# Performance work log

Hardware: AMD Instinct MI355X
Metric: run time of the kernel (lower is better)

Reference implementation:

```python
import jax, jax.numpy as jnp
import numpy as np

HEAD, SIZE = 16, 64
DIM = HEAD * SIZE
NINF = -10000.0
EPS = 1e-6


def setup_inputs() -> dict:
    key = jax.random.key(0)
    ks = jax.random.split(key, 12)
    B, S = 4, 2048
    std = 0.02
    return {
        "x": jax.random.normal(ks[0], (B, S, DIM), jnp.float32),
        "mask": jax.random.randint(ks[1], (B, S), 0, 2, jnp.int32),
        "wq_w": jax.random.normal(ks[2], (DIM, DIM), jnp.float32) * std,
        "wq_b": jnp.zeros((DIM,), jnp.float32),
        "wk_w": jax.random.normal(ks[3], (DIM, DIM), jnp.float32) * std,
        "wk_b": jnp.zeros((DIM,), jnp.float32),
        "wv_w": jax.random.normal(ks[4], (DIM, DIM), jnp.float32) * std,
        "wv_b": jnp.zeros((DIM,), jnp.float32),
        "dense_w": jax.random.normal(ks[5], (DIM, DIM), jnp.float32) * std,
        "dense_b": jnp.zeros((DIM,), jnp.float32),
        "gamma": jnp.ones((DIM,), jnp.float32),
        "beta": jnp.zeros((DIM,), jnp.float32),
    }


def _split_heads(t):
    # [B, S, DIM] -> [B, H, S, size]
    B, S, _ = t.shape
    return t.reshape(B, S, HEAD, SIZE).transpose(0, 2, 1, 3)


def _layernorm(x, gamma, beta):
    mu = jnp.mean(x, axis=-1, keepdims=True)
    var = jnp.mean(jnp.square(x - mu), axis=-1, keepdims=True)
    return (x - mu) * jax.lax.rsqrt(var + EPS) * gamma + beta


def reference(x, mask, wq_w, wq_b, wk_w, wk_b, wv_w, wv_b, dense_w, dense_b, gamma, beta):
    B, S, _ = x.shape
    q = _split_heads(x @ wq_w + wq_b)
    k = _split_heads(x @ wk_w + wk_b)
    v = _split_heads(x @ wv_w + wv_b)
    # scores [B, H, S, S]
    scores = jnp.einsum("bhqd,bhkd->bhqk", q, k) / jnp.sqrt(jnp.float32(SIZE))
    scores = scores + mask.astype(jnp.float32)[:, None, None, :] * NINF
    attn = jax.nn.softmax(scores, axis=-1)
    ctx = jnp.einsum("bhqk,bhkd->bhqd", attn, v)  # [B, H, S, size]
    ctx = ctx.transpose(0, 2, 1, 3).reshape(B, S, DIM)
    out = _layernorm(x + (ctx @ dense_w + dense_b), gamma, beta)
    return out, attn
```

## Files before the change

kernel.cpp:

```cpp
#include <hip/hip_runtime.h>
#include <stdint.h>

#define NB 4
#define NS 2048
#define NH 16
#define HSZ 64
#define ND 1024
#define NM (NB*NS)
#define QSCALE 0.180336880f
#define MADD2 -14426.950409f

typedef unsigned short u16;
typedef unsigned int u32;
typedef __attribute__((ext_vector_type(4))) float f32x4;
typedef __attribute__((ext_vector_type(8))) __bf16 bf16x8;

static __device__ __forceinline__ u16 f2bf(float f){
  unsigned int x = __builtin_bit_cast(unsigned int, f);
  x += 0x7fffu + ((x >> 16) & 1u);
  return (u16)(x >> 16);
}
static __device__ __forceinline__ u16 f2bf_rz(float f){
  return (u16)(__builtin_bit_cast(unsigned int, f) >> 16);
}

#define GLDS16(gp, lp) __builtin_amdgcn_global_load_lds( \
    (const __attribute__((address_space(1))) void*)(gp),  \
    (__attribute__((address_space(3))) void*)(lp), 16, 0, 0)

__global__ __launch_bounds__(256) void k_cast(const float4* __restrict__ in,
                                              ushort4* __restrict__ out, int n4){
  int i = blockIdx.x*256 + threadIdx.x;
  if (i >= n4) return;
  float4 v = in[i];
  ushort4 o;
  o.x = f2bf(v.x); o.y = f2bf(v.y); o.z = f2bf(v.z); o.w = f2bf(v.w);
  out[i] = o;
}

__global__ __launch_bounds__(256) void k_transpose4(const float* __restrict__ wq,
    const float* __restrict__ wk, const float* __restrict__ wv,
    const float* __restrict__ wd, u16* __restrict__ wcat, u16* __restrict__ wdt){
  __shared__ float t[32][33];
  const int z = blockIdx.z;
  const float* in = (z==0) ? wq : (z==1) ? wk : (z==2) ? wv : wd;
  u16* out = (z<3) ? (wcat + (size_t)z*ND*ND) : wdt;
  int tx = threadIdx.x & 31, ty = threadIdx.x >> 5;
  int n0 = blockIdx.x*32, k0 = blockIdx.y*32;
  #pragma unroll
  for (int i=0;i<32;i+=8)
    t[ty+i][tx] = in[(size_t)(k0+ty+i)*ND + n0 + tx];
  __syncthreads();
  #pragma unroll
  for (int i=0;i<32;i+=8)
    out[(size_t)(n0+ty+i)*ND + k0 + tx] = f2bf(t[tx][ty+i]);
}

template<int EPI>
__global__ __launch_bounds__(256,2) void k_gemm(const u16* __restrict__ A,
    const u16* __restrict__ Bt, const float* __restrict__ b0,
    const float* __restrict__ b1, const float* __restrict__ b2,
    const float* __restrict__ resid, u16* __restrict__ Qo, u16* __restrict__ Ko,
    u16* __restrict__ Vto, float* __restrict__ Out){
  __shared__ u16 sA[128*64];
  __shared__ u16 sB[128*64];
  const int tid = threadIdx.x;
  const int wave = tid >> 6, lane = tid & 63;
  const int l15 = lane & 15, l4 = lane >> 4;
  const int m0 = blockIdx.x * 128, n0 = blockIdx.y * 128;
  const int wm = wave >> 1, wn = wave & 1;
  const f32x4 vz = {0.f,0.f,0.f,0.f};
  f32x4 acc[4][4];
  #pragma unroll
  for (int i=0;i<4;i++)
    #pragma unroll
    for (int j=0;j<4;j++) acc[i][j] = vz;

  for (int k0 = 0; k0 < 1024; k0 += 64){
    __syncthreads();
    #pragma unroll
    for (int t=0; t<4; t++){
      const int jb = (t*4 + wave)*64;
      const int j  = jb + lane;
      const int r = j >> 3, c = (j & 7) << 3;
      GLDS16(A  + (((size_t)(m0 + r)) << 10) + (size_t)(k0 + c), sA + jb*8);
      GLDS16(Bt + (((size_t)(n0 + r)) << 10) + (size_t)(k0 + c), sB + jb*8);
    }
    __syncthreads();
    #pragma unroll
    for (int kk=0; kk<64; kk+=32){
      bf16x8 af[4], bv[4];
      #pragma unroll
      for (int mi=0;mi<4;mi++)
        af[mi] = *(const bf16x8*)(const void*)(sA + (wm*64 + mi*16 + l15)*64 + kk + l4*8);
      #pragma unroll
      for (int ni=0;ni<4;ni++)
        bv[ni] = *(const bf16x8*)(const void*)(sB + (wn*64 + ni*16 + l15)*64 + kk + l4*8);
      #pragma unroll
      for (int mi=0;mi<4;mi++)
        #pragma unroll
        for (int ni=0;ni<4;ni++)
          acc[mi][ni] = __builtin_amdgcn_mfma_f32_16x16x32_bf16(af[mi], bv[ni], acc[mi][ni], 0, 0, 0);
    }
  }

  if (EPI == 0){
    const int sec = n0 >> 10;
    const float* bias = (sec==0) ? b0 : (sec==1) ? b1 : b2;
    const float scale = (sec==0) ? QSCALE : 1.0f;
    u16* dst = (sec==0) ? Qo : (sec==1) ? Ko : Vto;
    #pragma unroll
    for (int mi=0;mi<4;mi++){
      #pragma unroll
      for (int ni=0;ni<4;ni++){
        const int n = n0 + wn*64 + ni*16 + l15;
        const int nn = n & (ND-1);
        const int h = nn >> 6, d = nn & 63;
        const float bvv = bias[nn];
        #pragma unroll
        for (int j=0;j<4;j++){
          const int m = m0 + wm*64 + mi*16 + l4*4 + j;
          const int b = m >> 11, s = m & (NS-1);
          const float v = (acc[mi][ni][j] + bvv) * scale;
          if (sec < 2)
            dst[((((size_t)b*NH + h)*NS + s) << 6) + d] = f2bf(v);
          else
            dst[((((size_t)b*NH + h)*HSZ + d) << 11) + s] = f2bf(v);
        }
      }
    }
  } else {
    #pragma unroll
    for (int mi=0;mi<4;mi++){
      #pragma unroll
      for (int ni=0;ni<4;ni++){
        const int n = n0 + wn*64 + ni*16 + l15;
        const float bvv = b0[n];
        #pragma unroll
        for (int j=0;j<4;j++){
          const int m = m0 + wm*64 + mi*16 + l4*4 + j;
          const size_t o = ((size_t)m << 10) + n;
          Out[o] = acc[mi][ni][j] + bvv + resid[o];
        }
      }
    }
  }
}

static __device__ __forceinline__ void attn_decode(int bid, int& qb, int& bh){
  const int x = bid & 7, t = bid >> 3;
  qb = t & 15;
  bh = (t >> 4) * 8 + x;
}
static __device__ __forceinline__ void attn_decode8(int bid, int& qb, int& bh){
  const int x = bid & 7, t = bid >> 3;
  qb = t & 7;
  bh = (t >> 3) * 8 + x;
}

__global__ __launch_bounds__(512,4) void k_attn_stats(const u16* __restrict__ Q,
    const u16* __restrict__ K, const int* __restrict__ mask,
    float* __restrict__ stats){
  __shared__ u16 sK[2][64][72];
  __shared__ float sMadd[NS];
  const int tid = threadIdx.x, wave = tid>>6, lane = tid&63;
  const int l15 = lane&15, l4 = lane>>4;
  int qb, bh; attn_decode8(blockIdx.x, qb, bh);
  const int b = bh >> 4;
  const size_t hoff = (size_t)bh * NS * HSZ;
  const int q0 = qb*256 + wave*32;
  const u16* Kg = K + hoff;
  bf16x8 qf0[2], qf1[2];
  #pragma unroll
  for (int m=0;m<2;m++){
    qf0[m] = *(const bf16x8*)(const void*)(Q + hoff + (size_t)(q0+m*16+l15)*HSZ + l4*8);
    qf1[m] = *(const bf16x8*)(const void*)(Q + hoff + (size_t)(q0+m*16+l15)*HSZ + 32 + l4*8);
  }
  const f32x4 vz = {0.f,0.f,0.f,0.f};
  const int r = tid >> 3, c = (tid & 7) << 3;
  float lr[2][4] = {{0.f,0.f,0.f,0.f},{0.f,0.f,0.f,0.f}};

  #pragma unroll
  for (int t=0;t<4;t++){
    const int kk = t*512 + tid;
    sMadd[kk] = mask[b*NS + kk] ? MADD2 : 0.f;
  }
  int4 rK = *(const int4*)(const void*)(Kg + (size_t)r*HSZ + c);
  *(int4*)(void*)&sK[0][r][c] = rK;
  rK = *(const int4*)(const void*)(Kg + (size_t)(64+r)*HSZ + c);
  __syncthreads();

  for (int kb=0; kb<NS; kb+=64){
    const int cur = (kb>>6)&1;
    if (kb+64 < NS)
      *(int4*)(void*)&sK[cur^1][r][c] = rK;
    if (kb+128 < NS)
      rK = *(const int4*)(const void*)(Kg + (size_t)(kb+128+r)*HSZ + c);
    #pragma unroll
    for (int n=0;n<4;n++){
      bf16x8 kf0 = *(const bf16x8*)(const void*)&sK[cur][n*16+l15][l4*8];
      bf16x8 kf1 = *(const bf16x8*)(const void*)&sK[cur][n*16+l15][32+l4*8];
      const float madd = sMadd[kb + n*16 + l15];
      #pragma unroll
      for (int m=0;m<2;m++){
        f32x4 a = vz;
        a = __builtin_amdgcn_mfma_f32_16x16x32_bf16(qf0[m], kf0, a, 0,0,0);
        a = __builtin_amdgcn_mfma_f32_16x16x32_bf16(qf1[m], kf1, a, 0,0,0);
        #pragma unroll
        for (int j=0;j<4;j++)
          lr[m][j] += __builtin_amdgcn_exp2f(a[j] + madd);
      }
    }
    __syncthreads();
  }
  #pragma unroll
  for (int m=0;m<2;m++)
    #pragma unroll
    for (int j=0;j<4;j++){
      float l = lr[m][j];
      #pragma unroll
      for (int off=1; off<16; off<<=1)
        l += __shfl_xor(l, off, 64);
      if (l15 == 0)
        stats[(size_t)bh*NS + q0 + m*16 + l4*4 + j] = 1.f/l;
    }
}

__global__ __launch_bounds__(512,4) void k_attn_pv(const u16* __restrict__ Q,
    const u16* __restrict__ K, const u16* __restrict__ Vt,
    const int* __restrict__ mask, const float* __restrict__ stats,
    float* __restrict__ attn, u16* __restrict__ ctx){
  __shared__ u16 sK[2][64][72];
  __shared__ u16 sV[2][64][72];
  __shared__ u16 sP[8][16][72];
  __shared__ float sMadd[NS];
  const int tid = threadIdx.x, wave = tid>>6, lane = tid&63;
  const int l15 = lane&15, l4 = lane>>4;
  int qb, bh; attn_decode(blockIdx.x, qb, bh);
  const int b = bh >> 4, h = bh & 15;
  const size_t hoff = (size_t)bh * NS * HSZ;
  const int q0 = qb*128 + wave*16;
  const u16* Kg = K + hoff;
  const u16* Vg = Vt + hoff;
  const bf16x8 qf0 = *(const bf16x8*)(const void*)(Q + hoff + (size_t)(q0+l15)*HSZ + l4*8);
  const bf16x8 qf1 = *(const bf16x8*)(const void*)(Q + hoff + (size_t)(q0+l15)*HSZ + 32 + l4*8);
  float rinv[4];
  #pragma unroll
  for (int j=0;j<4;j++)
    rinv[j] = stats[(size_t)bh*NS + q0 + l4*4 + j];
  const f32x4 vz = {0.f,0.f,0.f,0.f};
  f32x4 cacc[4];
  #pragma unroll
  for (int i=0;i<4;i++) cacc[i] = vz;
  float* attn_base = attn + (size_t)bh * NS * NS;
  const int r = tid >> 3, c = (tid & 7) << 3;

  #pragma unroll
  for (int t=0;t<4;t++){
    const int kk = t*512 + tid;
    sMadd[kk] = mask[b*NS + kk] ? MADD2 : 0.f;
  }
  int4 rK = *(const int4*)(const void*)(Kg + (size_t)r*HSZ + c);
  int4 rV = *(const int4*)(const void*)(Vg + (size_t)r*NS + c);
  *(int4*)(void*)&sK[0][r][c] = rK;
  *(int4*)(void*)&sV[0][r][c] = rV;
  rK = *(const int4*)(const void*)(Kg + (size_t)(64+r)*HSZ + c);
  rV = *(const int4*)(const void*)(Vg + (size_t)r*NS + 64 + c);
  __syncthreads();

  for (int kb=0; kb<NS; kb+=64){
    const int cur = (kb>>6)&1;
    if (kb+64 < NS){
      *(int4*)(void*)&sK[cur^1][r][c] = rK;
      *(int4*)(void*)&sV[cur^1][r][c] = rV;
    }
    if (kb+128 < NS){
      rK = *(const int4*)(const void*)(Kg + (size_t)(kb+128+r)*HSZ + c);
      rV = *(const int4*)(const void*)(Vg + (size_t)r*NS + (kb+128) + c);
    }
    #pragma unroll
    for (int n=0;n<4;n++){
      bf16x8 kf0 = *(const bf16x8*)(const void*)&sK[cur][n*16+l15][l4*8];
      bf16x8 kf1 = *(const bf16x8*)(const void*)&sK[cur][n*16+l15][32+l4*8];
      f32x4 a = vz;
      a = __builtin_amdgcn_mfma_f32_16x16x32_bf16(qf0, kf0, a, 0,0,0);
      a = __builtin_amdgcn_mfma_f32_16x16x32_bf16(qf1, kf1, a, 0,0,0);
      const float madd = sMadd[kb + n*16 + l15];
      #pragma unroll
      for (int j=0;j<4;j++){
        const float e = __builtin_amdgcn_exp2f(a[j] + madd);
        sP[wave][l4*4+j][n*16+l15] = f2bf_rz(e * rinv[j]);
      }
    }
    #pragma unroll
    for (int kk=0;kk<2;kk++){
      bf16x8 pf = *(const bf16x8*)(const void*)&sP[wave][l15][kk*32 + l4*8];
      #pragma unroll
      for (int n2=0;n2<4;n2++){
        bf16x8 vf = *(const bf16x8*)(const void*)&sV[cur][n2*16+l15][kk*32 + l4*8];
        cacc[n2] = __builtin_amdgcn_mfma_f32_16x16x32_bf16(pf, vf, cacc[n2], 0,0,0);
      }
    }
    #pragma unroll
    for (int jj=0;jj<4;jj++){
      const int rr = jj*4 + l4;
      const uint2 pw = *(const uint2*)(const void*)&sP[wave][rr][l15*4];
      f32x4 o;
      o.x = __builtin_bit_cast(float, pw.x << 16);
      o.y = __builtin_bit_cast(float, pw.x & 0xffff0000u);
      o.z = __builtin_bit_cast(float, pw.y << 16);
      o.w = __builtin_bit_cast(float, pw.y & 0xffff0000u);
      __builtin_nontemporal_store(o,
          (f32x4*)(void*)&attn_base[(size_t)(q0 + rr)*NS + kb + l15*4]);
    }
    __syncthreads();
  }
  #pragma unroll
  for (int n2=0;n2<4;n2++)
    #pragma unroll
    for (int j=0;j<4;j++){
      const int q = q0 + l4*4 + j;
      ctx[(((size_t)(b*NS + q)) << 10) + h*HSZ + n2*16 + l15] = f2bf(cacc[n2][j]);
    }
}

__global__ __launch_bounds__(256) void k_layernorm(float* __restrict__ buf,
    const float* __restrict__ gamma, const float* __restrict__ beta){
  const int row = blockIdx.x, tid = threadIdx.x;
  float4* rp = (float4*)(buf + ((size_t)row << 10));
  float4 a = rp[tid];
  float s  = a.x + a.y + a.z + a.w;
  float ss = a.x*a.x + a.y*a.y + a.z*a.z + a.w*a.w;
  #pragma unroll
  for (int off=1; off<64; off<<=1){
    s  += __shfl_xor(s,  off, 64);
    ss += __shfl_xor(ss, off, 64);
  }
  __shared__ float red[8];
  const int wave = tid>>6, lane = tid&63;
  if (lane == 0){ red[wave] = s; red[wave+4] = ss; }
  __syncthreads();
  s  = red[0]+red[1]+red[2]+red[3];
  ss = red[4]+red[5]+red[6]+red[7];
  const float mu  = s * (1.f/1024.f);
  const float var = ss * (1.f/1024.f) - mu*mu;
  const float rs  = rsqrtf(var + 1e-6f);
  float4 g  = ((const float4*)gamma)[tid];
  float4 be = ((const float4*)beta)[tid];
  float4 o;
  o.x = (a.x-mu)*rs*g.x + be.x;
  o.y = (a.y-mu)*rs*g.y + be.y;
  o.z = (a.z-mu)*rs*g.z + be.z;
  o.w = (a.w-mu)*rs*g.w + be.w;
  rp[tid] = o;
}

extern "C" void kernel_launch(void* const* d_in, const int* in_sizes, int n_in,
                              void* d_out, int out_size, void* d_ws, size_t ws_size,
                              hipStream_t stream){
  const float* x     = (const float*)d_in[0];
  const int*   mask  = (const int*)d_in[1];
  const float* wq_w  = (const float*)d_in[2];
  const float* wq_b  = (const float*)d_in[3];
  const float* wk_w  = (const float*)d_in[4];
  const float* wk_b  = (const float*)d_in[5];
  const float* wv_w  = (const float*)d_in[6];
  const float* wv_b  = (const float*)d_in[7];
  const float* wd_w  = (const float*)d_in[8];
  const float* wd_b  = (const float*)d_in[9];
  const float* gamma = (const float*)d_in[10];
  const float* beta  = (const float*)d_in[11];

  float* out0 = (float*)d_out;
  float* attn = out0 + (size_t)NM * ND;

  char* ws = (char*)d_ws;
  u16*   xb    = (u16*)(ws);
  u16*   ctx   = (u16*)(ws);
  u16*   wcat  = (u16*)(ws + (16u<<20));
  u16*   wdt   = (u16*)(ws + (22u<<20));
  u16*   Qb    = (u16*)(ws + (24u<<20));
  u16*   Kb    = (u16*)(ws + (40u<<20));
  u16*   Vtb   = (u16*)(ws + (56u<<20));
  float* stats = (float*)(ws + (72u<<20));

  k_cast<<<8192, 256, 0, stream>>>((const float4*)x, (ushort4*)xb, NM*ND/4);
  k_transpose4<<<dim3(32,32,4), 256, 0, stream>>>(wq_w, wk_w, wv_w, wd_w, wcat, wdt);

  k_gemm<0><<<dim3(64,24), 256, 0, stream>>>(xb, wcat, wq_b, wk_b, wv_b,
                                             nullptr, Qb, Kb, Vtb, nullptr);

  k_attn_stats<<<512, 512, 0, stream>>>(Qb, Kb, mask, stats);
  k_attn_pv<<<1024, 512, 0, stream>>>(Qb, Kb, Vtb, mask, stats, attn, ctx);

  k_gemm<2><<<dim3(64,8), 256, 0, stream>>>(ctx, wdt, wd_b, nullptr, nullptr,
                                            x, nullptr, nullptr, nullptr, out0);
  k_layernorm<<<NM, 256, 0, stream>>>(out0, gamma, beta);
}
```

Baseline: 412.9 us.

## Load K and V fragments directly from global memory, drop LDS staging and barriers

After: 733.5 us. +77.7%, slower.

```diff
diff --git a/kernel.cpp b/kernel.cpp
--- a/kernel.cpp
+++ b/kernel.cpp
@@ -161,7 +161,6 @@
 __global__ __launch_bounds__(512,4) void k_attn_stats(const u16* __restrict__ Q,
     const u16* __restrict__ K, const int* __restrict__ mask,
     float* __restrict__ stats){
-  __shared__ u16 sK[2][64][72];
   __shared__ float sMadd[NS];
   const int tid = threadIdx.x, wave = tid>>6, lane = tid&63;
   const int l15 = lane&15, l4 = lane>>4;
@@ -177,7 +176,6 @@
     qf1[m] = *(const bf16x8*)(const void*)(Q + hoff + (size_t)(q0+m*16+l15)*HSZ + 32 + l4*8);
   }
   const f32x4 vz = {0.f,0.f,0.f,0.f};
-  const int r = tid >> 3, c = (tid & 7) << 3;
   float lr[2][4] = {{0.f,0.f,0.f,0.f},{0.f,0.f,0.f,0.f}};
 
   #pragma unroll
@@ -185,33 +183,29 @@
     const int kk = t*512 + tid;
     sMadd[kk] = mask[b*NS + kk] ? MADD2 : 0.f;
   }
-  int4 rK = *(const int4*)(const void*)(Kg + (size_t)r*HSZ + c);
-  *(int4*)(void*)&sK[0][r][c] = rK;
-  rK = *(const int4*)(const void*)(Kg + (size_t)(64+r)*HSZ + c);
   __syncthreads();
 
   for (int kb=0; kb<NS; kb+=64){
-    const int cur = (kb>>6)&1;
-    if (kb+64 < NS)
-      *(int4*)(void*)&sK[cur^1][r][c] = rK;
-    if (kb+128 < NS)
-      rK = *(const int4*)(const void*)(Kg + (size_t)(kb+128+r)*HSZ + c);
+    bf16x8 kf[4][2];
     #pragma unroll
     for (int n=0;n<4;n++){
-      bf16x8 kf0 = *(const bf16x8*)(const void*)&sK[cur][n*16+l15][l4*8];
-      bf16x8 kf1 = *(const bf16x8*)(const void*)&sK[cur][n*16+l15][32+l4*8];
+      const u16* kp = Kg + (size_t)(kb + n*16 + l15)*HSZ + l4*8;
+      kf[n][0] = *(const bf16x8*)(const void*)(kp);
+      kf[n][1] = *(const bf16x8*)(const void*)(kp + 32);
+    }
+    #pragma unroll
+    for (int n=0;n<4;n++){
       const float madd = sMadd[kb + n*16 + l15];
       #pragma unroll
       for (int m=0;m<2;m++){
         f32x4 a = vz;
-        a = __builtin_amdgcn_mfma_f32_16x16x32_bf16(qf0[m], kf0, a, 0,0,0);
-        a = __builtin_amdgcn_mfma_f32_16x16x32_bf16(qf1[m], kf1, a, 0,0,0);
+        a = __builtin_amdgcn_mfma_f32_16x16x32_bf16(qf0[m], kf[n][0], a, 0,0,0);
+        a = __builtin_amdgcn_mfma_f32_16x16x32_bf16(qf1[m], kf[n][1], a, 0,0,0);
         #pragma unroll
         for (int j=0;j<4;j++)
           lr[m][j] += __builtin_amdgcn_exp2f(a[j] + madd);
       }
     }
-    __syncthreads();
   }
   #pragma unroll
   for (int m=0;m<2;m++)
@@ -230,8 +224,6 @@
     const u16* __restrict__ K, const u16* __restrict__ Vt,
     const int* __restrict__ mask, const float* __restrict__ stats,
     float* __restrict__ attn, u16* __restrict__ ctx){
-  __shared__ u16 sK[2][64][72];
-  __shared__ u16 sV[2][64][72];
   __shared__ u16 sP[8][16][72];
   __shared__ float sMadd[NS];
   const int tid = threadIdx.x, wave = tid>>6, lane = tid&63;
@@ -253,38 +245,27 @@
   #pragma unroll
   for (int i=0;i<4;i++) cacc[i] = vz;
   float* attn_base = attn + (size_t)bh * NS * NS;
-  const int r = tid >> 3, c = (tid & 7) << 3;
 
   #pragma unroll
   for (int t=0;t<4;t++){
     const int kk = t*512 + tid;
     sMadd[kk] = mask[b*NS + kk] ? MADD2 : 0.f;
   }
-  int4 rK = *(const int4*)(const void*)(Kg + (size_t)r*HSZ + c);
-  int4 rV = *(const int4*)(const void*)(Vg + (size_t)r*NS + c);
-  *(int4*)(void*)&sK[0][r][c] = rK;
-  *(int4*)(void*)&sV[0][r][c] = rV;
-  rK = *(const int4*)(const void*)(Kg + (size_t)(64+r)*HSZ + c);
-  rV = *(const int4*)(const void*)(Vg + (size_t)r*NS + 64 + c);
   __syncthreads();
 
   for (int kb=0; kb<NS; kb+=64){
-    const int cur = (kb>>6)&1;
-    if (kb+64 < NS){
-      *(int4*)(void*)&sK[cur^1][r][c] = rK;
-      *(int4*)(void*)&sV[cur^1][r][c] = rV;
-    }
-    if (kb+128 < NS){
-      rK = *(const int4*)(const void*)(Kg + (size_t)(kb+128+r)*HSZ + c);
-      rV = *(const int4*)(const void*)(Vg + (size_t)r*NS + (kb+128) + c);
-    }
+    bf16x8 kf[4][2];
     #pragma unroll
     for (int n=0;n<4;n++){
-      bf16x8 kf0 = *(const bf16x8*)(const void*)&sK[cur][n*16+l15][l4*8];
-      bf16x8 kf1 = *(const bf16x8*)(const void*)&sK[cur][n*16+l15][32+l4*8];
+      const u16* kp = Kg + (size_t)(kb + n*16 + l15)*HSZ + l4*8;
+      kf[n][0] = *(const bf16x8*)(const void*)(kp);
+      kf[n][1] = *(const bf16x8*)(const void*)(kp + 32);
+    }
+    #pragma unroll
+    for (int n=0;n<4;n++){
       f32x4 a = vz;
-      a = __builtin_amdgcn_mfma_f32_16x16x32_bf16(qf0, kf0, a, 0,0,0);
-      a = __builtin_amdgcn_mfma_f32_16x16x32_bf16(qf1, kf1, a, 0,0,0);
+      a = __builtin_amdgcn_mfma_f32_16x16x32_bf16(qf0, kf[n][0], a, 0,0,0);
+      a = __builtin_amdgcn_mfma_f32_16x16x32_bf16(qf1, kf[n][1], a, 0,0,0);
       const float madd = sMadd[kb + n*16 + l15];
       #pragma unroll
       for (int j=0;j<4;j++){
@@ -297,7 +278,8 @@
       bf16x8 pf = *(const bf16x8*)(const void*)&sP[wave][l15][kk*32 + l4*8];
       #pragma unroll
       for (int n2=0;n2<4;n2++){
-        bf16x8 vf = *(const bf16x8*)(const void*)&sV[cur][n2*16+l15][kk*32 + l4*8];
+        bf16x8 vf = *(const bf16x8*)(const void*)
+            (Vg + (size_t)(n2*16+l15)*NS + kb + kk*32 + l4*8);
         cacc[n2] = __builtin_amdgcn_mfma_f32_16x16x32_bf16(pf, vf, cacc[n2], 0,0,0);
       }
     }
@@ -313,7 +295,6 @@
       __builtin_nontemporal_store(o,
           (f32x4*)(void*)&attn_base[(size_t)(q0 + rr)*NS + kb + l15*4]);
     }
-    __syncthreads();
   }
   #pragma unroll
   for (int n2=0;n2<4;n2++)
```
